# Kernel tuning notes

Measured on AMD Instinct MI355X. Metric: run time of the kernel, lower is better.

Reference implementation:

```python
import jax, jax.numpy as jnp
import numpy as np

N = 100000          # num_nodes
E = 1_600_000       # num_edges
F = 16              # node_features
HID = 32            # DCRNN hidden size (hardcoded in DCRNNModel)
OUT = 12            # output_len
K = 2               # diffusion steps (intended DCRNN; see notes)
CIN = F + HID       # DConv input channels: concat([X, H])


def setup_inputs() -> dict:
    key = jax.random.key(0)
    ks = jax.random.split(key, 12)
    x = jax.random.normal(ks[0], (N, F), dtype=jnp.float32)
    edge_index = jax.random.randint(ks[1], (2, E), 0, N, dtype=jnp.int32)
    edge_weight = jax.random.uniform(ks[2], (E,), jnp.float32, minval=0.05, maxval=1.0)
    sc = 0.1
    W_z = jax.random.normal(ks[3], (2, K, CIN, HID), jnp.float32) * sc
    b_z = jax.random.normal(ks[4], (HID,), jnp.float32) * sc
    W_r = jax.random.normal(ks[5], (2, K, CIN, HID), jnp.float32) * sc
    b_r = jax.random.normal(ks[6], (HID,), jnp.float32) * sc
    W_h = jax.random.normal(ks[7], (2, K, CIN, HID), jnp.float32) * sc
    b_h = jax.random.normal(ks[8], (HID,), jnp.float32) * sc
    lin_W = jax.random.normal(ks[9], (HID, OUT), jnp.float32) * sc
    lin_b = jax.random.normal(ks[10], (OUT,), jnp.float32) * sc
    return {"x": x, "edge_index": edge_index, "edge_weight": edge_weight,
            "W_z": W_z, "b_z": b_z, "W_r": W_r, "b_r": b_r,
            "W_h": W_h, "b_h": b_h, "lin_W": lin_W, "lin_b": lin_b}


def reference(x, edge_index, edge_weight, W_z, b_z, W_r, b_r, W_h, b_h, lin_W, lin_b):
    src, dst = edge_index[0], edge_index[1]
    # weighted out/in degrees (as in to_dense_adj row/col sums)
    deg_out = jax.ops.segment_sum(edge_weight, src, num_segments=N)
    deg_in = jax.ops.segment_sum(edge_weight, dst, num_segments=N)
    inv_out_e = (1.0 / deg_out)[src][:, None]  # [E,1] per-edge 1/deg_out(src)
    inv_in_e = (1.0 / deg_in)[dst][:, None]    # [E,1] per-edge 1/deg_in(dst)

    def dconv(Xc, W, b):
        # K=0 term (both diffusion directions share Tx_0 = X)
        H = Xc @ W[0, 0] + Xc @ W[1, 0]
        # forward diffusion: out[dst] += (1/deg_out[src]) * Xc[src]
        T_o = jax.ops.segment_sum(inv_out_e * Xc[src], dst, num_segments=N)
        # reverse diffusion: out[src] += (1/deg_in[dst]) * Xc[dst]
        T_i = jax.ops.segment_sum(inv_in_e * Xc[dst], src, num_segments=N)
        return H + T_o @ W[0, 1] + T_i @ W[1, 1] + b

    H0 = jnp.zeros((N, HID), dtype=x.dtype)
    XH = jnp.concatenate([x, H0], axis=1)           # [N, F+HID]
    Z = jax.nn.sigmoid(dconv(XH, W_z, b_z))         # update gate
    R = jax.nn.sigmoid(dconv(XH, W_r, b_r))         # reset gate
    XHr = jnp.concatenate([x, H0 * R], axis=1)
    H_tilde = jnp.tanh(dconv(XHr, W_h, b_h))
    H = Z * H0 + (1.0 - Z) * H_tilde                # [N, HID]
    return jax.nn.relu(H) @ lin_W + lin_b           # [N, OUT]
```

## Files before the change

### kernel.cpp

```cpp
#include <hip/hip_runtime.h>
#include <math.h>

#define N_NODES 100000
#define N_EDGES 1600000
#define NF 16
#define HID 32
#define OUTD 12
#define CIN3 48

#define NB   1024
#define RNG  98
#define PBLK 256
#define PT   1024
#define CHUNK ((N_EDGES + PBLK - 1) / PBLK)
#define CAP   2560
#define CAPT  10
#define ACCN  7

typedef unsigned int uint;


__global__ __launch_bounds__(PT)
void p1_count(const int* __restrict__ ei, uint* __restrict__ cntD, uint* __restrict__ cntS) {
    __shared__ uint cD[NB], cS[NB];
    int t = threadIdx.x, blk = blockIdx.x;
    for (int i = t; i < NB; i += PT) { cD[i] = 0; cS[i] = 0; }
    __syncthreads();
    int lo = blk * CHUNK, hi = min(lo + CHUNK, N_EDGES);
    for (int e = lo + t; e < hi; e += PT) {
        uint s = (uint)ei[e];
        uint d = (uint)ei[N_EDGES + e];
        atomicAdd(&cS[s / RNG], 1u);
        atomicAdd(&cD[d / RNG], 1u);
    }
    __syncthreads();
    for (int i = t; i < NB; i += PT) {
        cntD[i * PBLK + blk] = cD[i];
        cntS[i * PBLK + blk] = cS[i];
    }
}

__global__ __launch_bounds__(256)
void p2a_rowsum(const uint* __restrict__ cntD, const uint* __restrict__ cntS,
                uint* __restrict__ totD, uint* __restrict__ totS) {
    __shared__ uint red[256];
    int t = threadIdx.x;
    bool isS = blockIdx.x >= NB;
    int b = isS ? (blockIdx.x - NB) : blockIdx.x;
    const uint* cnt = isS ? cntS : cntD;
    red[t] = cnt[b * PBLK + t];
    __syncthreads();
    for (int s = 128; s > 0; s >>= 1) { if (t < s) red[t] += red[t + s]; __syncthreads(); }
    if (t == 0) (isS ? totS : totD)[b] = red[0];
}

__global__ __launch_bounds__(256)
void p2b_scan(const uint* __restrict__ totD, const uint* __restrict__ totS,
              uint* __restrict__ baseD, uint* __restrict__ baseS) {
    __shared__ uint part[256];
    int t = threadIdx.x;
    for (int dir = 0; dir < 2; ++dir) {
        const uint* tot = dir ? totS : totD;
        uint* base = dir ? baseS : baseD;
        uint v[4]; uint s = 0;
#pragma unroll
        for (int k = 0; k < 4; ++k) { v[k] = tot[t * 4 + k]; s += v[k]; }
        part[t] = s;
        __syncthreads();
        if (t == 0) {
            uint a = 0;
            for (int k = 0; k < 256; ++k) { uint x = part[k]; part[k] = a; a += x; }
            base[NB] = a;
        }
        __syncthreads();
        uint a = part[t];
#pragma unroll
        for (int k = 0; k < 4; ++k) { base[t * 4 + k] = a; a += v[k]; }
        __syncthreads();
    }
}

__global__ __launch_bounds__(256)
void p2c_rowscan(const uint* __restrict__ cntD, const uint* __restrict__ cntS,
                 const uint* __restrict__ baseD, const uint* __restrict__ baseS,
                 uint* __restrict__ offD, uint* __restrict__ offS) {
    __shared__ uint row[PBLK];
    int t = threadIdx.x;
    bool isS = blockIdx.x >= NB;
    int b = isS ? (blockIdx.x - NB) : blockIdx.x;
    const uint* cnt = isS ? cntS : cntD;
    const uint* base = isS ? baseS : baseD;
    uint* off = isS ? offS : offD;
    row[t] = cnt[b * PBLK + t];
    __syncthreads();
    if (t == 0) {
        uint a = base[b];
        for (int k = 0; k < PBLK; ++k) { uint v = row[k]; row[k] = a; a += v; }
    }
    __syncthreads();
    off[b * PBLK + t] = row[t];
}

__global__ __launch_bounds__(PT)
void p3_scatter(const int* __restrict__ ei, const float* __restrict__ ew,
                const uint* __restrict__ cntD, const uint* __restrict__ cntS,
                const uint* __restrict__ offD, const uint* __restrict__ offS,
                uint* __restrict__ recXD, uint* __restrict__ recWD,
                uint* __restrict__ recXS, uint* __restrict__ recWS) {
    __shared__ uint sorted[CHUNK];
    __shared__ uint sbuf[NB];
    __shared__ uint cstart[NB];
    __shared__ uint scur[NB];
    int t = threadIdx.x, blk = blockIdx.x;
    int lo = blk * CHUNK, hi = min(lo + CHUNK, N_EDGES);
    int n = hi - lo;

    for (int dir = 0; dir < 2; ++dir) {
        const uint* cnt = dir ? cntS : cntD;
        const uint* off = dir ? offS : offD;
        uint* recX      = dir ? recXS : recXD;
        uint* recW      = dir ? recWS : recWD;
        const int* own  = dir ? ei : (ei + N_EDGES);
        uint v = cnt[t * PBLK + blk];
        sbuf[t] = v;
        __syncthreads();
        for (int d = 1; d < NB; d <<= 1) {
            uint a = (t >= d) ? sbuf[t - d] : 0u;
            __syncthreads();
            sbuf[t] += a;
            __syncthreads();
        }
        cstart[t] = sbuf[t] - v;
        scur[t]   = sbuf[t] - v;
        __syncthreads();
        sbuf[t] = off[t * PBLK + blk];
        for (int i = t; i < n; i += PT) {
            uint b = (uint)own[lo + i] / RNG;
            uint p = atomicAdd(&scur[b], 1u);
            sorted[p] = (b << 13) | (uint)i;
        }
        __syncthreads();
        for (int i = t; i < n; i += PT) {
            uint v2 = sorted[i];
            uint b = v2 >> 13;
            int e = lo + (int)(v2 & 8191u);
            uint s  = (uint)ei[e];
            uint d2 = (uint)ei[N_EDGES + e];
            uint wfix = (uint)(ew[e] * 16777216.0f + 0.5f);
            uint ownode = dir ? s : d2;
            uint other  = dir ? d2 : s;
            uint lcl  = ownode - b * RNG;
            uint gpos = sbuf[b] + (i - cstart[b]);
            recX[gpos] = other | (lcl << 20);
            recW[gpos] = (lcl << 25) | wfix;
        }
        __syncthreads();
    }
}

__global__ __launch_bounds__(256)
void kdeg(const uint* __restrict__ recWD, const uint* __restrict__ recWS,
          const uint* __restrict__ baseD, const uint* __restrict__ baseS,
          float* __restrict__ inv_in, float* __restrict__ inv_out) {
    __shared__ uint dacc[RNG];
    int t = threadIdx.x;
    bool isS = blockIdx.x >= NB;
    int b = isS ? (blockIdx.x - NB) : blockIdx.x;
    const uint* rec = isS ? recWS : recWD;
    const uint* base = isS ? baseS : baseD;
    float* inv = isS ? inv_out : inv_in;
    for (int i = t; i < RNG; i += 256) dacc[i] = 0u;
    __syncthreads();
    uint lo = base[b], hi = base[b + 1];
    for (uint e = lo + t; e < hi; e += 256) {
        uint r = rec[e];
        atomicAdd(&dacc[r >> 25], r & 0x1FFFFFFu);
    }
    __syncthreads();
    int n0 = b * RNG;
    for (int i = t; i < RNG; i += 256) {
        int n = n0 + i;
        if (n < N_NODES) inv[n] = 16777216.0f / (float)dacc[i];
    }
}

__global__ __launch_bounds__(256)
void p4_sorted(const uint* __restrict__ recXD, const uint* __restrict__ recXS,
               const uint* __restrict__ baseD, const uint* __restrict__ baseS,
               const float* __restrict__ x,
               const float* __restrict__ inv_out, const float* __restrict__ inv_in,
               float* __restrict__ To, float* __restrict__ Ti) {
    __shared__ uint sorted[CAP];
    __shared__ uint scnt[RNG];
    __shared__ uint cstart[RNG + 1];
    __shared__ uint scur[RNG];
    int t = threadIdx.x;
    bool isS = blockIdx.x >= NB;
    int b = isS ? (blockIdx.x - NB) : blockIdx.x;
    const uint* rec = isS ? recXS : recXD;
    const uint* base = isS ? baseS : baseD;
    const float* inv = isS ? inv_in : inv_out;
    float* out = isS ? Ti : To;

    int f = t & 15, s = t >> 4;
    uint lo = base[b], hi = base[b + 1];

    float acc[ACCN];
#pragma unroll
    for (int k = 0; k < ACCN; ++k) acc[k] = 0.0f;

    for (uint chunk = lo; chunk < hi; chunk += CAP) {
        uint n_in = min(hi - chunk, (uint)CAP);
        for (int i = t; i < RNG; i += 256) scnt[i] = 0;
        __syncthreads();
        uint stash[CAPT];
#pragma unroll
        for (int k = 0; k < CAPT; ++k) {
            uint i = (uint)(k * 256 + t);
            if (i < n_in) {
                uint r = rec[chunk + i];
                stash[k] = r;
                atomicAdd(&scnt[r >> 20], 1u);
            }
        }
        __syncthreads();
        if (t == 0) {
            uint a = 0;
            for (int n = 0; n < RNG; ++n) { cstart[n] = a; a += scnt[n]; }
            cstart[RNG] = a;
        }
        __syncthreads();
        for (int i = t; i < RNG; i += 256) scur[i] = cstart[i];
        __syncthreads();
#pragma unroll
        for (int k = 0; k < CAPT; ++k) {
            uint i = (uint)(k * 256 + t);
            if (i < n_in) {
                uint r = stash[k];
                uint p = atomicAdd(&scur[r >> 20], 1u);
                sorted[p] = r;
            }
        }
        __syncthreads();
#pragma unroll
        for (int k = 0; k < ACCN; ++k) {
            int n = s + 16 * k;
            if (n < RNG) {
                uint j = cstart[n], j1 = cstart[n + 1];
                for (; j + 8 <= j1; j += 8) {
                    uint p0 = sorted[j],     p1 = sorted[j + 1], p2 = sorted[j + 2], p3 = sorted[j + 3];
                    uint p4 = sorted[j + 4], p5 = sorted[j + 5], p6 = sorted[j + 6], p7 = sorted[j + 7];
                    uint o0 = p0 & 0xFFFFFu, o1 = p1 & 0xFFFFFu, o2 = p2 & 0xFFFFFu, o3 = p3 & 0xFFFFFu;
                    uint o4 = p4 & 0xFFFFFu, o5 = p5 & 0xFFFFFu, o6 = p6 & 0xFFFFFu, o7 = p7 & 0xFFFFFu;
                    float g0 = x[(size_t)o0 * NF + f], g1 = x[(size_t)o1 * NF + f];
                    float g2 = x[(size_t)o2 * NF + f], g3 = x[(size_t)o3 * NF + f];
                    float g4 = x[(size_t)o4 * NF + f], g5 = x[(size_t)o5 * NF + f];
                    float g6 = x[(size_t)o6 * NF + f], g7 = x[(size_t)o7 * NF + f];
                    float w0 = inv[o0], w1 = inv[o1], w2 = inv[o2], w3 = inv[o3];
                    float w4 = inv[o4], w5 = inv[o5], w6 = inv[o6], w7 = inv[o7];
                    acc[k] += g0 * w0 + g1 * w1 + g2 * w2 + g3 * w3
                            + g4 * w4 + g5 * w5 + g6 * w6 + g7 * w7;
                }
                for (; j < j1; ++j) {
                    uint p = sorted[j];
                    uint o = p & 0xFFFFFu;
                    acc[k] += x[(size_t)o * NF + f] * inv[o];
                }
            }
        }
        __syncthreads();
    }

#pragma unroll
    for (int k = 0; k < ACCN; ++k) {
        int n = s + 16 * k;
        if (n < RNG) {
            size_t g = (size_t)b * RNG + n;
            if (g < N_NODES) out[g * NF + f] = acc[k];
        }
    }
}

__global__ void wprep_kernel(const float* __restrict__ Wz, const float* __restrict__ Wh,
                             float* __restrict__ WzT, float* __restrict__ WhT) {
    int t = blockIdx.x * blockDim.x + threadIdx.x;
    if (t >= 2 * CIN3 * HID) return;
    const float* W = (t < CIN3 * HID) ? Wz : Wh;
    float* WT      = (t < CIN3 * HID) ? WzT : WhT;
    int i = (t < CIN3 * HID) ? t : (t - CIN3 * HID);
    int c = i / HID;
    int h = i - c * HID;
    float v;
    if (c < 16)      v = W[(0 * 48 + c) * 32 + h] + W[(2 * 48 + c) * 32 + h];
    else if (c < 32) v = W[(1 * 48 + (c - 16)) * 32 + h];
    else             v = W[(3 * 48 + (c - 32)) * 32 + h];
    WT[h * CIN3 + c] = v;
}

__global__ __launch_bounds__(256)
void node_kernel(const float* __restrict__ x, const float* __restrict__ To,
                 const float* __restrict__ Ti,
                 const float* __restrict__ WzT, const float* __restrict__ WhT,
                 const float* __restrict__ bz, const float* __restrict__ bh,
                 const float* __restrict__ linW, const float* __restrict__ linb,
                 float* __restrict__ out) {
    __shared__ __align__(16) float sWz[HID * CIN3];
    __shared__ __align__(16) float sWh[HID * CIN3];
    __shared__ __align__(16) float sBz[HID], sBh[HID];
    __shared__ __align__(16) float sLW[HID * OUTD];
    __shared__ __align__(16) float sLb[OUTD];

    for (int i = threadIdx.x; i < HID * CIN3; i += 256) { sWz[i] = WzT[i]; sWh[i] = WhT[i]; }
    if (threadIdx.x < HID) { sBz[threadIdx.x] = bz[threadIdx.x]; sBh[threadIdx.x] = bh[threadIdx.x]; }
    for (int i = threadIdx.x; i < HID * OUTD; i += 256) sLW[i] = linW[i];
    if (threadIdx.x < OUTD) sLb[threadIdx.x] = linb[threadIdx.x];
    __syncthreads();

    int n = blockIdx.x * 256 + threadIdx.x;
    if (n >= N_NODES) return;

    float feat[CIN3];
#pragma unroll
    for (int q = 0; q < 4; ++q) {
        float4 v = ((const float4*)(x + (size_t)n * NF))[q];
        feat[q*4+0]=v.x; feat[q*4+1]=v.y; feat[q*4+2]=v.z; feat[q*4+3]=v.w;
    }
#pragma unroll
    for (int q = 0; q < 4; ++q) {
        float4 v = ((const float4*)(To + (size_t)n * NF))[q];
        feat[16+q*4+0]=v.x; feat[16+q*4+1]=v.y; feat[16+q*4+2]=v.z; feat[16+q*4+3]=v.w;
    }
#pragma unroll
    for (int q = 0; q < 4; ++q) {
        float4 v = ((const float4*)(Ti + (size_t)n * NF))[q];
        feat[32+q*4+0]=v.x; feat[32+q*4+1]=v.y; feat[32+q*4+2]=v.z; feat[32+q*4+3]=v.w;
    }

    float o[OUTD];
#pragma unroll
    for (int j = 0; j < OUTD; ++j) o[j] = sLb[j];

#pragma unroll 2
    for (int h = 0; h < HID; ++h) {
        float az = sBz[h];
        float ah = sBh[h];
        const float4* wz4 = (const float4*)(sWz + h * CIN3);
        const float4* wh4 = (const float4*)(sWh + h * CIN3);
#pragma unroll
        for (int q = 0; q < CIN3 / 4; ++q) {
            float4 wz = wz4[q];
            float4 wh = wh4[q];
            float f0 = feat[q*4+0], f1 = feat[q*4+1], f2 = feat[q*4+2], f3 = feat[q*4+3];
            az += f0*wz.x + f1*wz.y + f2*wz.z + f3*wz.w;
            ah += f0*wh.x + f1*wh.y + f2*wh.z + f3*wh.w;
        }
        float z  = 1.0f / (1.0f + expf(-az));
        float ht = tanhf(ah);
        float r  = fmaxf((1.0f - z) * ht, 0.0f);
#pragma unroll
        for (int j = 0; j < OUTD; ++j) o[j] += r * sLW[h * OUTD + j];
    }

    float4* op = (float4*)(out + (size_t)n * OUTD);
    op[0] = make_float4(o[0], o[1], o[2],  o[3]);
    op[1] = make_float4(o[4], o[5], o[6],  o[7]);
    op[2] = make_float4(o[8], o[9], o[10], o[11]);
}

__global__ void zero_kernel(float* __restrict__ p, int n) {
    int i = blockIdx.x * blockDim.x + threadIdx.x;
    int stride = gridDim.x * blockDim.x;
    for (; i < n; i += stride) p[i] = 0.0f;
}
__global__ void degree_compact(const int* __restrict__ ei, const float* __restrict__ ew,
                               float* __restrict__ deg_out, float* __restrict__ deg_in) {
    int e = blockIdx.x * blockDim.x + threadIdx.x;
    if (e >= N_EDGES) return;
    atomicAdd(&deg_out[ei[e]], ew[e]);
    atomicAdd(&deg_in[ei[N_EDGES + e]], ew[e]);
}
__global__ void rcp_compact(float* __restrict__ a, float* __restrict__ b) {
    int n = blockIdx.x * blockDim.x + threadIdx.x;
    if (n >= N_NODES) return;
    a[n] = 1.0f / a[n]; b[n] = 1.0f / b[n];
}
__global__ __launch_bounds__(256)
void scatter_kernel(const int* __restrict__ ei, const float* __restrict__ x,
                    const float* __restrict__ inv_out, const float* __restrict__ inv_in,
                    float* __restrict__ To, float* __restrict__ Ti) {
    int t = blockIdx.x * blockDim.x + threadIdx.x;
    if (t >= N_EDGES * NF) return;
    int e = t >> 4, f = t & 15;
    int src = ei[e], dst = ei[N_EDGES + e];
    atomicAdd(&To[dst * NF + f], x[src * NF + f] * inv_out[src]);
    atomicAdd(&Ti[src * NF + f], x[dst * NF + f] * inv_in[dst]);
}

extern "C" void kernel_launch(void* const* d_in, const int* in_sizes, int n_in,
                              void* d_out, int out_size, void* d_ws, size_t ws_size,
                              hipStream_t stream) {
    const float* x    = (const float*)d_in[0];
    const int*   ei   = (const int*)  d_in[1];
    const float* ew   = (const float*)d_in[2];
    const float* Wz   = (const float*)d_in[3];
    const float* bz   = (const float*)d_in[4];
    const float* Wh   = (const float*)d_in[7];
    const float* bh   = (const float*)d_in[8];
    const float* linW = (const float*)d_in[9];
    const float* linb = (const float*)d_in[10];

    float* ws = (float*)d_ws;

    size_t off = 0;
    uint* recXD = (uint*)(ws + off);  off += (size_t)N_EDGES;
    uint* recWD = (uint*)(ws + off);  off += (size_t)N_EDGES;
    uint* recXS = (uint*)(ws + off);  off += (size_t)N_EDGES;
    uint* recWS = (uint*)(ws + off);  off += (size_t)N_EDGES;
    uint* cntD  = (uint*)(ws + off);  off += (size_t)NB * PBLK;
    uint* cntS  = (uint*)(ws + off);  off += (size_t)NB * PBLK;
    uint* offD  = (uint*)(ws + off);  off += (size_t)NB * PBLK;
    uint* offS  = (uint*)(ws + off);  off += (size_t)NB * PBLK;
    uint* totD  = (uint*)(ws + off);  off += NB;
    uint* totS  = (uint*)(ws + off);  off += NB;
    uint* baseD = (uint*)(ws + off);  off += NB + 1;
    uint* baseS = (uint*)(ws + off);  off += NB + 1;
    float* inv_out = ws + off;        off += N_NODES;
    float* inv_in  = ws + off;        off += N_NODES;
    float* To   = ws + off;           off += (size_t)NF * N_NODES;
    float* Ti   = ws + off;           off += (size_t)NF * N_NODES;
    float* WzT  = ws + off;           off += CIN3 * HID;
    float* WhT  = ws + off;           off += CIN3 * HID;
    size_t need = off * sizeof(float);

    if (ws_size >= need) {
        p1_count    <<<PBLK,  PT,  0, stream>>>(ei, cntD, cntS);
        p2a_rowsum  <<<2*NB,  256, 0, stream>>>(cntD, cntS, totD, totS);
        p2b_scan    <<<1,     256, 0, stream>>>(totD, totS, baseD, baseS);
        p2c_rowscan <<<2*NB,  256, 0, stream>>>(cntD, cntS, baseD, baseS, offD, offS);
        p3_scatter  <<<PBLK,  PT,  0, stream>>>(ei, ew, cntD, cntS, offD, offS,
                                                recXD, recWD, recXS, recWS);
        kdeg        <<<2*NB,  256, 0, stream>>>(recWD, recWS, baseD, baseS, inv_in, inv_out);
        wprep_kernel<<<12,    256, 0, stream>>>(Wz, Wh, WzT, WhT);
        p4_sorted   <<<2*NB,  256, 0, stream>>>(recXD, recXS, baseD, baseS, x, inv_out, inv_in, To, Ti);
        node_kernel <<<(N_NODES + 255) / 256, 256, 0, stream>>>(x, To, Ti, WzT, WhT, bz, bh,
                                                                linW, linb, (float*)d_out);
    } else {
        float* fTo  = ws;
        float* fTi  = ws + 16 * N_NODES;
        float* fIo  = ws + 32 * N_NODES;
        float* fIi  = ws + 33 * N_NODES;
        float* fWzT = ws + 34 * N_NODES;
        float* fWhT = fWzT + CIN3 * HID;
        zero_kernel<<<2048, 256, 0, stream>>>(fTo, 34 * N_NODES);
        degree_compact<<<(N_EDGES + 255) / 256, 256, 0, stream>>>(ei, ew, fIo, fIi);
        rcp_compact<<<(N_NODES + 255) / 256, 256, 0, stream>>>(fIo, fIi);
        scatter_kernel<<<(N_EDGES * NF + 255) / 256, 256, 0, stream>>>(ei, x, fIo, fIi, fTo, fTi);
        wprep_kernel<<<12, 256, 0, stream>>>(Wz, Wh, fWzT, fWhT);
        node_kernel<<<(N_NODES + 255) / 256, 256, 0, stream>>>(x, fTo, fTi, fWzT, fWhT, bz, bh,
                                                               linW, linb, (float*)d_out);
    }
}
```

Measured before the change: 164.5 us.

## Fuse sorted diffusion gather with node GRU/linear epilogue per bucket

Merges the per-bucket sorted gather kernel and the node-wise gate/linear kernel into one kernel. Each block now processes both diffusion directions for its node range, keeps the To/Ti results in shared memory, and then computes the GRU update and output projection directly. This removes the global To/Ti round trip and one launch, but halves the grid to 1024 blocks doing both directions serially, and only 98 of 256 threads take part in the epilogue.

```diff
diff --git a/kernel.cpp b/kernel.cpp
--- a/kernel.cpp
+++ b/kernel.cpp
@@ -16,6 +16,8 @@
 #define CAP   2560
 #define CAPT  10
 #define ACCN  7
+#define TILE  1668
+#define TBLOB 8536
 
 typedef unsigned int uint;
 
@@ -181,103 +183,6 @@
     for (int i = t; i < RNG; i += 256) {
         int n = n0 + i;
         if (n < N_NODES) inv[n] = 16777216.0f / (float)dacc[i];
-    }
-}
-
-__global__ __launch_bounds__(256)
-void p4_sorted(const uint* __restrict__ recXD, const uint* __restrict__ recXS,
-               const uint* __restrict__ baseD, const uint* __restrict__ baseS,
-               const float* __restrict__ x,
-               const float* __restrict__ inv_out, const float* __restrict__ inv_in,
-               float* __restrict__ To, float* __restrict__ Ti) {
-    __shared__ uint sorted[CAP];
-    __shared__ uint scnt[RNG];
-    __shared__ uint cstart[RNG + 1];
-    __shared__ uint scur[RNG];
-    int t = threadIdx.x;
-    bool isS = blockIdx.x >= NB;
-    int b = isS ? (blockIdx.x - NB) : blockIdx.x;
-    const uint* rec = isS ? recXS : recXD;
-    const uint* base = isS ? baseS : baseD;
-    const float* inv = isS ? inv_in : inv_out;
-    float* out = isS ? Ti : To;
-
-    int f = t & 15, s = t >> 4;
-    uint lo = base[b], hi = base[b + 1];
-
-    float acc[ACCN];
-#pragma unroll
-    for (int k = 0; k < ACCN; ++k) acc[k] = 0.0f;
-
-    for (uint chunk = lo; chunk < hi; chunk += CAP) {
-        uint n_in = min(hi - chunk, (uint)CAP);
-        for (int i = t; i < RNG; i += 256) scnt[i] = 0;
-        __syncthreads();
-        uint stash[CAPT];
-#pragma unroll
-        for (int k = 0; k < CAPT; ++k) {
-            uint i = (uint)(k * 256 + t);
-            if (i < n_in) {
-                uint r = rec[chunk + i];
-                stash[k] = r;
-                atomicAdd(&scnt[r >> 20], 1u);
-            }
-        }
-        __syncthreads();
-        if (t == 0) {
-            uint a = 0;
-            for (int n = 0; n < RNG; ++n) { cstart[n] = a; a += scnt[n]; }
-            cstart[RNG] = a;
-        }
-        __syncthreads();
-        for (int i = t; i < RNG; i += 256) scur[i] = cstart[i];
-        __syncthreads();
-#pragma unroll
-        for (int k = 0; k < CAPT; ++k) {
-            uint i = (uint)(k * 256 + t);
-            if (i < n_in) {
-                uint r = stash[k];
-                uint p = atomicAdd(&scur[r >> 20], 1u);
-                sorted[p] = r;
-            }
-        }
-        __syncthreads();
-#pragma unroll
-        for (int k = 0; k < ACCN; ++k) {
-            int n = s + 16 * k;
-            if (n < RNG) {
-                uint j = cstart[n], j1 = cstart[n + 1];
-                for (; j + 8 <= j1; j += 8) {
-                    uint p0 = sorted[j],     p1 = sorted[j + 1], p2 = sorted[j + 2], p3 = sorted[j + 3];
-                    uint p4 = sorted[j + 4], p5 = sorted[j + 5], p6 = sorted[j + 6], p7 = sorted[j + 7];
-                    uint o0 = p0 & 0xFFFFFu, o1 = p1 & 0xFFFFFu, o2 = p2 & 0xFFFFFu, o3 = p3 & 0xFFFFFu;
-                    uint o4 = p4 & 0xFFFFFu, o5 = p5 & 0xFFFFFu, o6 = p6 & 0xFFFFFu, o7 = p7 & 0xFFFFFu;
-                    float g0 = x[(size_t)o0 * NF + f], g1 = x[(size_t)o1 * NF + f];
-                    float g2 = x[(size_t)o2 * NF + f], g3 = x[(size_t)o3 * NF + f];
-                    float g4 = x[(size_t)o4 * NF + f], g5 = x[(size_t)o5 * NF + f];
-                    float g6 = x[(size_t)o6 * NF + f], g7 = x[(size_t)o7 * NF + f];
-                    float w0 = inv[o0], w1 = inv[o1], w2 = inv[o2], w3 = inv[o3];
-                    float w4 = inv[o4], w5 = inv[o5], w6 = inv[o6], w7 = inv[o7];
-                    acc[k] += g0 * w0 + g1 * w1 + g2 * w2 + g3 * w3
-                            + g4 * w4 + g5 * w5 + g6 * w6 + g7 * w7;
-                }
-                for (; j < j1; ++j) {
-                    uint p = sorted[j];
-                    uint o = p & 0xFFFFFu;
-                    acc[k] += x[(size_t)o * NF + f] * inv[o];
-                }
-            }
-        }
-        __syncthreads();
-    }
-
-#pragma unroll
-    for (int k = 0; k < ACCN; ++k) {
-        int n = s + 16 * k;
-        if (n < RNG) {
-            size_t g = (size_t)b * RNG + n;
-            if (g < N_NODES) out[g * NF + f] = acc[k];
-        }
     }
 }
 
@@ -298,6 +203,195 @@
 }
 
 __global__ __launch_bounds__(256)
+void p4node(const uint* __restrict__ recXD, const uint* __restrict__ recXS,
+            const uint* __restrict__ baseD, const uint* __restrict__ baseS,
+            const float* __restrict__ x,
+            const float* __restrict__ inv_out, const float* __restrict__ inv_in,
+            const float* __restrict__ WzT, const float* __restrict__ WhT,
+            const float* __restrict__ bz, const float* __restrict__ bh,
+            const float* __restrict__ linW, const float* __restrict__ linb,
+            float* __restrict__ out) {
+    __shared__ __align__(16) uint blob[TBLOB];
+    float* tTo   = (float*)blob;
+    float* tTi   = (float*)(blob + TILE);
+    uint*  sorted = blob + 2 * TILE;
+    uint*  scnt   = blob + 2 * TILE + CAP;
+    uint*  cstart = scnt + RNG;
+    uint*  scur   = cstart + RNG + 1;
+    float* xt  = (float*)(blob + 2 * TILE);
+    float* sWz = (float*)(blob + 2 * TILE + TILE);
+    float* sWh = (float*)(blob + 2 * TILE + TILE + 1536);
+    float* sBz = (float*)(blob + 8076);
+    float* sBh = (float*)(blob + 8108);
+    float* sLW = (float*)(blob + 8140);
+    float* sLb = (float*)(blob + 8524);
+
+    int t = threadIdx.x, b = blockIdx.x;
+    int f = t & 15, s = t >> 4;
+
+#pragma unroll
+    for (int dir = 0; dir < 2; ++dir) {
+        const uint* rec  = dir ? recXS : recXD;
+        const uint* base = dir ? baseS : baseD;
+        const float* inv = dir ? inv_in : inv_out;
+        float* tile      = dir ? tTi : tTo;
+        uint lo = base[b], hi = base[b + 1];
+
+        float acc[ACCN];
+#pragma unroll
+        for (int k = 0; k < ACCN; ++k) acc[k] = 0.0f;
+
+        for (uint chunk = lo; chunk < hi; chunk += CAP) {
+            uint n_in = min(hi - chunk, (uint)CAP);
+            for (int i = t; i < RNG; i += 256) scnt[i] = 0;
+            __syncthreads();
+            uint stash[CAPT];
+#pragma unroll
+            for (int k = 0; k < CAPT; ++k) {
+                uint i = (uint)(k * 256 + t);
+                if (i < n_in) {
+                    uint r = rec[chunk + i];
+                    stash[k] = r;
+                    atomicAdd(&scnt[r >> 20], 1u);
+                }
+            }
+            __syncthreads();
+            if (t == 0) {
+                uint a = 0;
+                for (int n = 0; n < RNG; ++n) { cstart[n] = a; a += scnt[n]; }
+                cstart[RNG] = a;
+            }
+            __syncthreads();
+            for (int i = t; i < RNG; i += 256) scur[i] = cstart[i];
+            __syncthreads();
+#pragma unroll
+            for (int k = 0; k < CAPT; ++k) {
+                uint i = (uint)(k * 256 + t);
+                if (i < n_in) {
+                    uint r = stash[k];
+                    uint p = atomicAdd(&scur[r >> 20], 1u);
+                    sorted[p] = r;
+                }
+            }
+            __syncthreads();
+#pragma unroll
+            for (int k = 0; k < ACCN; ++k) {
+                int n = s + 16 * k;
+                if (n < RNG) {
+                    uint j = cstart[n], j1 = cstart[n + 1];
+                    for (; j + 8 <= j1; j += 8) {
+                        uint p0 = sorted[j],     p1 = sorted[j + 1], p2 = sorted[j + 2], p3 = sorted[j + 3];
+                        uint p4 = sorted[j + 4], p5 = sorted[j + 5], p6 = sorted[j + 6], p7 = sorted[j + 7];
+                        uint o0 = p0 & 0xFFFFFu, o1 = p1 & 0xFFFFFu, o2 = p2 & 0xFFFFFu, o3 = p3 & 0xFFFFFu;
+                        uint o4 = p4 & 0xFFFFFu, o5 = p5 & 0xFFFFFu, o6 = p6 & 0xFFFFFu, o7 = p7 & 0xFFFFFu;
+                        float g0 = x[(size_t)o0 * NF + f], g1 = x[(size_t)o1 * NF + f];
+                        float g2 = x[(size_t)o2 * NF + f], g3 = x[(size_t)o3 * NF + f];
+                        float g4 = x[(size_t)o4 * NF + f], g5 = x[(size_t)o5 * NF + f];
+                        float g6 = x[(size_t)o6 * NF + f], g7 = x[(size_t)o7 * NF + f];
+                        float w0 = inv[o0], w1 = inv[o1], w2 = inv[o2], w3 = inv[o3];
+                        float w4 = inv[o4], w5 = inv[o5], w6 = inv[o6], w7 = inv[o7];
+                        acc[k] += g0 * w0 + g1 * w1 + g2 * w2 + g3 * w3
+                                + g4 * w4 + g5 * w5 + g6 * w6 + g7 * w7;
+                    }
+                    for (; j < j1; ++j) {
+                        uint p = sorted[j];
+                        uint o = p & 0xFFFFFu;
+                        acc[k] += x[(size_t)o * NF + f] * inv[o];
+                    }
+                }
+            }
+            __syncthreads();
+        }
+#pragma unroll
+        for (int k = 0; k < ACCN; ++k) {
+            int n = s + 16 * k;
+            if (n < RNG) tile[n * 17 + f] = acc[k];
+        }
+    }
+
+    for (int i = t; i < RNG * NF; i += 256) {
+        int g = b * RNG * NF + i;
+        xt[(i >> 4) * 17 + (i & 15)] = (g < N_NODES * NF) ? x[g] : 0.0f;
+    }
+    for (int i = t; i < HID * CIN3; i += 256) { sWz[i] = WzT[i]; sWh[i] = WhT[i]; }
+    if (t < HID) { sBz[t] = bz[t]; sBh[t] = bh[t]; }
+    for (int i = t; i < HID * OUTD; i += 256) sLW[i] = linW[i];
+    if (t < OUTD) sLb[t] = linb[t];
+    __syncthreads();
+
+    if (t < RNG) {
+        size_t g = (size_t)b * RNG + t;
+        if (g < N_NODES) {
+            float feat[CIN3];
+#pragma unroll
+            for (int c = 0; c < NF; ++c) feat[c]      = xt[t * 17 + c];
+#pragma unroll
+            for (int c = 0; c < NF; ++c) feat[16 + c] = tTo[t * 17 + c];
+#pragma unroll
+            for (int c = 0; c < NF; ++c) feat[32 + c] = tTi[t * 17 + c];
+
+            float o[OUTD];
+#pragma unroll
+            for (int j = 0; j < OUTD; ++j) o[j] = sLb[j];
+
+#pragma unroll 2
+            for (int h = 0; h < HID; ++h) {
+                float az = sBz[h];
+                float ah = sBh[h];
+                const float4* wz4 = (const float4*)(sWz + h * CIN3);
+                const float4* wh4 = (const float4*)(sWh + h * CIN3);
+#pragma unroll
+                for (int q = 0; q < CIN3 / 4; ++q) {
+                    float4 wz = wz4[q];
+                    float4 wh = wh4[q];
+                    float f0 = feat[q*4+0], f1 = feat[q*4+1], f2 = feat[q*4+2], f3 = feat[q*4+3];
+                    az += f0*wz.x + f1*wz.y + f2*wz.z + f3*wz.w;
+                    ah += f0*wh.x + f1*wh.y + f2*wh.z + f3*wh.w;
+                }
+                float z  = 1.0f / (1.0f + expf(-az));
+                float ht = tanhf(ah);
+                float r  = fmaxf((1.0f - z) * ht, 0.0f);
+#pragma unroll
+                for (int j = 0; j < OUTD; ++j) o[j] += r * sLW[h * OUTD + j];
+            }
+
+            float4* op = (float4*)(out + g * OUTD);
+            op[0] = make_float4(o[0], o[1], o[2],  o[3]);
+            op[1] = make_float4(o[4], o[5], o[6],  o[7]);
+            op[2] = make_float4(o[8], o[9], o[10], o[11]);
+        }
+    }
+}
+
+__global__ void zero_kernel(float* __restrict__ p, int n) {
+    int i = blockIdx.x * blockDim.x + threadIdx.x;
+    int stride = gridDim.x * blockDim.x;
+    for (; i < n; i += stride) p[i] = 0.0f;
+}
+__global__ void degree_compact(const int* __restrict__ ei, const float* __restrict__ ew,
+                               float* __restrict__ deg_out, float* __restrict__ deg_in) {
+    int e = blockIdx.x * blockDim.x + threadIdx.x;
+    if (e >= N_EDGES) return;
+    atomicAdd(&deg_out[ei[e]], ew[e]);
+    atomicAdd(&deg_in[ei[N_EDGES + e]], ew[e]);
+}
+__global__ void rcp_compact(float* __restrict__ a, float* __restrict__ b) {
+    int n = blockIdx.x * blockDim.x + threadIdx.x;
+    if (n >= N_NODES) return;
+    a[n] = 1.0f / a[n]; b[n] = 1.0f / b[n];
+}
+__global__ __launch_bounds__(256)
+void scatter_kernel(const int* __restrict__ ei, const float* __restrict__ x,
+                    const float* __restrict__ inv_out, const float* __restrict__ inv_in,
+                    float* __restrict__ To, float* __restrict__ Ti) {
+    int t = blockIdx.x * blockDim.x + threadIdx.x;
+    if (t >= N_EDGES * NF) return;
+    int e = t >> 4, f = t & 15;
+    int src = ei[e], dst = ei[N_EDGES + e];
+    atomicAdd(&To[dst * NF + f], x[src * NF + f] * inv_out[src]);
+    atomicAdd(&Ti[src * NF + f], x[dst * NF + f] * inv_in[dst]);
+}
+__global__ __launch_bounds__(256)
 void node_kernel(const float* __restrict__ x, const float* __restrict__ To,
                  const float* __restrict__ Ti,
                  const float* __restrict__ WzT, const float* __restrict__ WhT,
@@ -365,35 +459,6 @@
     op[0] = make_float4(o[0], o[1], o[2],  o[3]);
     op[1] = make_float4(o[4], o[5], o[6],  o[7]);
     op[2] = make_float4(o[8], o[9], o[10], o[11]);
-}
-
-__global__ void zero_kernel(float* __restrict__ p, int n) {
-    int i = blockIdx.x * blockDim.x + threadIdx.x;
-    int stride = gridDim.x * blockDim.x;
-    for (; i < n; i += stride) p[i] = 0.0f;
-}
-__global__ void degree_compact(const int* __restrict__ ei, const float* __restrict__ ew,
-                               float* __restrict__ deg_out, float* __restrict__ deg_in) {
-    int e = blockIdx.x * blockDim.x + threadIdx.x;
-    if (e >= N_EDGES) return;
-    atomicAdd(&deg_out[ei[e]], ew[e]);
-    atomicAdd(&deg_in[ei[N_EDGES + e]], ew[e]);
-}
-__global__ void rcp_compact(float* __restrict__ a, float* __restrict__ b) {
-    int n = blockIdx.x * blockDim.x + threadIdx.x;
-    if (n >= N_NODES) return;
-    a[n] = 1.0f / a[n]; b[n] = 1.0f / b[n];
-}
-__global__ __launch_bounds__(256)
-void scatter_kernel(const int* __restrict__ ei, const float* __restrict__ x,
-                    const float* __restrict__ inv_out, const float* __restrict__ inv_in,
-                    float* __restrict__ To, float* __restrict__ Ti) {
-    int t = blockIdx.x * blockDim.x + threadIdx.x;
-    if (t >= N_EDGES * NF) return;
-    int e = t >> 4, f = t & 15;
-    int src = ei[e], dst = ei[N_EDGES + e];
-    atomicAdd(&To[dst * NF + f], x[src * NF + f] * inv_out[src]);
-    atomicAdd(&Ti[src * NF + f], x[dst * NF + f] * inv_in[dst]);
 }
 
 extern "C" void kernel_launch(void* const* d_in, const int* in_sizes, int n_in,
@@ -426,8 +491,6 @@
     uint* baseS = (uint*)(ws + off);  off += NB + 1;
     float* inv_out = ws + off;        off += N_NODES;
     float* inv_in  = ws + off;        off += N_NODES;
-    float* To   = ws + off;           off += (size_t)NF * N_NODES;
-    float* Ti   = ws + off;           off += (size_t)NF * N_NODES;
     float* WzT  = ws + off;           off += CIN3 * HID;
     float* WhT  = ws + off;           off += CIN3 * HID;
     size_t need = off * sizeof(float);
@@ -441,9 +504,9 @@
                                                 recXD, recWD, recXS, recWS);
         kdeg        <<<2*NB,  256, 0, stream>>>(recWD, recWS, baseD, baseS, inv_in, inv_out);
         wprep_kernel<<<12,    256, 0, stream>>>(Wz, Wh, WzT, WhT);
-        p4_sorted   <<<2*NB,  256, 0, stream>>>(recXD, recXS, baseD, baseS, x, inv_out, inv_in, To, Ti);
-        node_kernel <<<(N_NODES + 255) / 256, 256, 0, stream>>>(x, To, Ti, WzT, WhT, bz, bh,
-                                                                linW, linb, (float*)d_out);
+        p4node      <<<NB,    256, 0, stream>>>(recXD, recXS, baseD, baseS, x,
+                                                inv_out, inv_in, WzT, WhT, bz, bh,
+                                                linW, linb, (float*)d_out);
     } else {
         float* fTo  = ws;
         float* fTi  = ws + 16 * N_NODES;
```

Measured after the change: 237.1 us. 1.44x slower.

## Replace per-bucket LDS counting sort with fixed-point shared-memory atomic accumulation

Applied to the files above, without the earlier changes.

The aggregation kernel no longer counting-sorts each bucket's edge records in LDS and then reduces per node. Each thread now reads records directly, gathers x times the inverse degree, and adds the product as a 2^20-scaled fixed-point integer into a per-bucket shared accumulator using integer atomics. This removes several barriers, the serial prefix scan and the sort passes, at the cost of heavy LDS atomic contention and fixed-point rounding error. It also risks overflow for large sums, and results no longer sum in a fixed order.

```diff
diff --git a/kernel.cpp b/kernel.cpp
--- a/kernel.cpp
+++ b/kernel.cpp
@@ -13,9 +13,6 @@
 #define PBLK 256
 #define PT   1024
 #define CHUNK ((N_EDGES + PBLK - 1) / PBLK)
-#define CAP   2560
-#define CAPT  10
-#define ACCN  7
 
 typedef unsigned int uint;
 
@@ -185,15 +182,12 @@
 }
 
 __global__ __launch_bounds__(256)
-void p4_sorted(const uint* __restrict__ recXD, const uint* __restrict__ recXS,
-               const uint* __restrict__ baseD, const uint* __restrict__ baseS,
-               const float* __restrict__ x,
-               const float* __restrict__ inv_out, const float* __restrict__ inv_in,
-               float* __restrict__ To, float* __restrict__ Ti) {
-    __shared__ uint sorted[CAP];
-    __shared__ uint scnt[RNG];
-    __shared__ uint cstart[RNG + 1];
-    __shared__ uint scur[RNG];
+void p4_fixed(const uint* __restrict__ recXD, const uint* __restrict__ recXS,
+              const uint* __restrict__ baseD, const uint* __restrict__ baseS,
+              const float* __restrict__ x,
+              const float* __restrict__ inv_out, const float* __restrict__ inv_in,
+              float* __restrict__ To, float* __restrict__ Ti) {
+    __shared__ uint dacc[RNG * NF];
     int t = threadIdx.x;
     bool isS = blockIdx.x >= NB;
     int b = isS ? (blockIdx.x - NB) : blockIdx.x;
@@ -201,84 +195,37 @@
     const uint* base = isS ? baseS : baseD;
     const float* inv = isS ? inv_in : inv_out;
     float* out = isS ? Ti : To;
-
-    int f = t & 15, s = t >> 4;
+    for (int i = t; i < RNG * NF; i += 256) dacc[i] = 0u;
+    __syncthreads();
     uint lo = base[b], hi = base[b + 1];
-
-    float acc[ACCN];
-#pragma unroll
-    for (int k = 0; k < ACCN; ++k) acc[k] = 0.0f;
-
-    for (uint chunk = lo; chunk < hi; chunk += CAP) {
-        uint n_in = min(hi - chunk, (uint)CAP);
-        for (int i = t; i < RNG; i += 256) scnt[i] = 0;
-        __syncthreads();
-        uint stash[CAPT];
-#pragma unroll
-        for (int k = 0; k < CAPT; ++k) {
-            uint i = (uint)(k * 256 + t);
-            if (i < n_in) {
-                uint r = rec[chunk + i];
-                stash[k] = r;
-                atomicAdd(&scnt[r >> 20], 1u);
-            }
-        }
-        __syncthreads();
-        if (t == 0) {
-            uint a = 0;
-            for (int n = 0; n < RNG; ++n) { cstart[n] = a; a += scnt[n]; }
-            cstart[RNG] = a;
-        }
-        __syncthreads();
-        for (int i = t; i < RNG; i += 256) scur[i] = cstart[i];
-        __syncthreads();
-#pragma unroll
-        for (int k = 0; k < CAPT; ++k) {
-            uint i = (uint)(k * 256 + t);
-            if (i < n_in) {
-                uint r = stash[k];
-                uint p = atomicAdd(&scur[r >> 20], 1u);
-                sorted[p] = r;
-            }
-        }
-        __syncthreads();
-#pragma unroll
-        for (int k = 0; k < ACCN; ++k) {
-            int n = s + 16 * k;
-            if (n < RNG) {
-                uint j = cstart[n], j1 = cstart[n + 1];
-                for (; j + 8 <= j1; j += 8) {
-                    uint p0 = sorted[j],     p1 = sorted[j + 1], p2 = sorted[j + 2], p3 = sorted[j + 3];
-                    uint p4 = sorted[j + 4], p5 = sorted[j + 5], p6 = sorted[j + 6], p7 = sorted[j + 7];
-                    uint o0 = p0 & 0xFFFFFu, o1 = p1 & 0xFFFFFu, o2 = p2 & 0xFFFFFu, o3 = p3 & 0xFFFFFu;
-                    uint o4 = p4 & 0xFFFFFu, o5 = p5 & 0xFFFFFu, o6 = p6 & 0xFFFFFu, o7 = p7 & 0xFFFFFu;
-                    float g0 = x[(size_t)o0 * NF + f], g1 = x[(size_t)o1 * NF + f];
-                    float g2 = x[(size_t)o2 * NF + f], g3 = x[(size_t)o3 * NF + f];
-                    float g4 = x[(size_t)o4 * NF + f], g5 = x[(size_t)o5 * NF + f];
-                    float g6 = x[(size_t)o6 * NF + f], g7 = x[(size_t)o7 * NF + f];
-                    float w0 = inv[o0], w1 = inv[o1], w2 = inv[o2], w3 = inv[o3];
-                    float w4 = inv[o4], w5 = inv[o5], w6 = inv[o6], w7 = inv[o7];
-                    acc[k] += g0 * w0 + g1 * w1 + g2 * w2 + g3 * w3
-                            + g4 * w4 + g5 * w5 + g6 * w6 + g7 * w7;
-                }
-                for (; j < j1; ++j) {
-                    uint p = sorted[j];
-                    uint o = p & 0xFFFFFu;
-                    acc[k] += x[(size_t)o * NF + f] * inv[o];
-                }
-            }
-        }
-        __syncthreads();
-    }
-
-#pragma unroll
-    for (int k = 0; k < ACCN; ++k) {
-        int n = s + 16 * k;
-        if (n < RNG) {
-            size_t g = (size_t)b * RNG + n;
-            if (g < N_NODES) out[g * NF + f] = acc[k];
-        }
-    }
+    int f = t & 15, g = t >> 4;
+    uint e = lo + g;
+    for (; e + 112 < hi; e += 128) {
+        uint r[8];
+#pragma unroll
+        for (int k = 0; k < 8; ++k) r[k] = rec[e + 16 * k];
+        float v[8];
+#pragma unroll
+        for (int k = 0; k < 8; ++k) {
+            uint o = r[k] & 0xFFFFFu;
+            v[k] = x[(size_t)o * NF + f] * inv[o];
+        }
+#pragma unroll
+        for (int k = 0; k < 8; ++k)
+            atomicAdd(&dacc[(r[k] >> 20) * NF + f],
+                      (uint)__float2int_rn(v[k] * 1048576.0f));
+    }
+    for (; e < hi; e += 16) {
+        uint r = rec[e];
+        uint o = r & 0xFFFFFu;
+        float v = x[(size_t)o * NF + f] * inv[o];
+        atomicAdd(&dacc[(r >> 20) * NF + f], (uint)__float2int_rn(v * 1048576.0f));
+    }
+    __syncthreads();
+    size_t o0 = (size_t)b * RNG * NF;
+    int lim = N_NODES * NF - (int)o0;
+    for (int i = t; i < RNG * NF; i += 256)
+        if (i < lim) out[o0 + i] = (float)(int)dacc[i] * (1.0f / 1048576.0f);
 }
 
 __global__ void wprep_kernel(const float* __restrict__ Wz, const float* __restrict__ Wh,
@@ -441,7 +388,8 @@
                                                 recXD, recWD, recXS, recWS);
         kdeg        <<<2*NB,  256, 0, stream>>>(recWD, recWS, baseD, baseS, inv_in, inv_out);
         wprep_kernel<<<12,    256, 0, stream>>>(Wz, Wh, WzT, WhT);
-        p4_sorted   <<<2*NB,  256, 0, stream>>>(recXD, recXS, baseD, baseS, x, inv_out, inv_in, To, Ti);
+        p4_fixed    <<<2*NB,  256, 0, stream>>>(recXD, recXS, baseD, baseS, x,
+                                                inv_out, inv_in, To, Ti);
         node_kernel <<<(N_NODES + 255) / 256, 256, 0, stream>>>(x, To, Ti, WzT, WhT, bz, bh,
                                                                 linW, linb, (float*)d_out);
     } else {
```

After: 162.3 us. About the same (-1.3%).
